# Optimization experiments

Measured on AMD Instinct MI355X. Metric: run time of the kernel, lower is better.

The kernel has to match this reference:

```python
import jax, jax.numpy as jnp
import numpy as np

BN_EPS = 1e-5
LRELU_SLOPE = 0.1
F = 512  # feature dim fixed by ReFineBlock/Fc_ClassBlock input_dim


def _bn_eval(x, gamma, beta, mean, var):
    # BatchNorm1d in eval mode (running stats); elementwise over feature dim
    return (x - mean) * (gamma / jnp.sqrt(var + BN_EPS)) + beta


def _lrelu(x):
    return jnp.where(x > 0, x, LRELU_SLOPE * x)


def setup_inputs() -> dict:
    key = jax.random.key(0)
    ks = jax.random.split(key, 16)
    B, P, G = 128, 1, 4
    d = jax.random.normal(ks[0], (B, B, P, G, F), dtype=jnp.float32)
    w = jax.random.uniform(ks[1], (B * G, B * G), dtype=jnp.float32)
    W1 = jax.random.normal(ks[2], (F, F), dtype=jnp.float32) * 0.04
    b1 = jnp.zeros((F,), dtype=jnp.float32)
    g1 = jnp.ones((F,), dtype=jnp.float32)
    beta1 = jnp.zeros((F,), dtype=jnp.float32)
    m1 = jax.random.normal(ks[3], (F,), dtype=jnp.float32) * 0.1
    v1 = jax.random.uniform(ks[4], (F,), jnp.float32, 0.5, 1.5)
    W2 = jax.random.normal(ks[5], (F, F), dtype=jnp.float32) * 0.04
    b2 = jnp.zeros((F,), dtype=jnp.float32)
    g2 = jnp.ones((F,), dtype=jnp.float32)
    beta2 = jnp.zeros((F,), dtype=jnp.float32)
    m2 = jax.random.normal(ks[6], (F,), dtype=jnp.float32) * 0.1
    v2 = jax.random.uniform(ks[7], (F,), jnp.float32, 0.5, 1.5)
    # Fc_ClassBlock.classifier: Dropout(eval=id) + Linear(512, 2)
    Wc = jax.random.normal(ks[8], (2, F), dtype=jnp.float32) * 0.001
    bc = jnp.zeros((2,), dtype=jnp.float32)
    return {"d": d, "w": w, "W1": W1, "b1": b1, "g1": g1, "beta1": beta1,
            "m1": m1, "v1": v1, "W2": W2, "b2": b2, "g2": g2, "beta2": beta2,
            "m2": m2, "v2": v2, "Wc": Wc, "bc": bc}


def reference(d, w, W1, b1, g1, beta1, m1, v1, W2, b2, g2, beta2, m2, v2, Wc, bc):
    batch_size = d.shape[1]          # len(d[0])
    num_g = d.shape[3]
    feat = d.shape[-1]
    N = batch_size * num_g           # adjacency size

    # Vectorized ReFineBlock over every (k, :, i, j) row (eval mode: dropout=id)
    x = d.reshape(-1, feat)
    h = _lrelu(_bn_eval(x @ W1.T + b1, g1, beta1, m1, v1))
    h = _lrelu(_bn_eval(h @ W2.T + b2, g2, beta2, m2, v2))
    t = h.reshape(batch_size, -1, feat)   # (B, B*G, F)

    # preprocess_adj: adj = w + I; D^{-1/2}; (adj @ D).T @ D
    adj = w.reshape(N, N) + jnp.eye(N, dtype=w.dtype)
    rowsum = adj.sum(axis=1)
    d_inv_sqrt = jnp.power(rowsum, -0.5)
    d_inv_sqrt = jnp.where(jnp.isinf(d_inv_sqrt), 0.0, d_inv_sqrt)
    w_norm = (adj * d_inv_sqrt[None, :]).T * d_inv_sqrt[None, :]  # (N, N)

    # GCN propagation: d_new[:, :, i] = t[:, :, i] @ w_norm for each feature i
    d_new = jnp.einsum('bmf,mn->bnf', t, w_norm)  # (B, N, F)

    # classifier.classifier (dropout=id + Linear) applied per probe row
    result = d_new @ Wc.T + bc  # (B, N, 2)
    return result.reshape(-1, 2)
```

## Files before the change

kernel.cpp:

```cpp
#include <hip/hip_runtime.h>
#include <hip/hip_bf16.h>


typedef __hip_bfloat16 bf16_t;
typedef __bf16 bf16x8 __attribute__((ext_vector_type(8)));
typedef __bf16 bf16x4 __attribute__((ext_vector_type(4)));
typedef float f32x4 __attribute__((ext_vector_type(4)));

#define KDIM 512
#define BM 64

__device__ __forceinline__ float ldsel(const void* p, int i, int isbf) {
    return isbf ? __bfloat162float(((const bf16_t*)p)[i]) : ((const float*)p)[i];
}

__global__ void probe_kernel(const void* __restrict__ d, int* __restrict__ flag) {
    const unsigned short* u = (const unsigned short*)d;
    const int l = threadIdx.x;
    int cnt = 0;
    for (int i = l; i < 256; i += 64) {
        const int e = (u[i] >> 7) & 0xFF;
        cnt += (e >= 118 && e <= 129) ? 1 : 0;
    }
    #pragma unroll
    for (int off = 32; off; off >>= 1) cnt += __shfl_down(cnt, off, 64);
    if (l == 0) *flag = (cnt >= 200) ? 1 : 0;
}

__global__ void rowsum_kernel(const void* __restrict__ w, const int* __restrict__ flagp,
                              float* __restrict__ dinv) {
    const int isbf = *flagp;
    const int i = blockIdx.x;
    const int l = threadIdx.x;
    float s = 0.f;
    for (int j = l; j < 512; j += 64) s += ldsel(w, i * 512 + j, isbf);
    #pragma unroll
    for (int off = 32; off; off >>= 1) s += __shfl_down(s, off, 64);
    if (l == 0) dinv[i] = 1.0f / sqrtf(s + 1.0f);
}

__global__ void params_kernel(const void* g1, const void* b1, const void* m1,
                              const void* v1, const void* be1,
                              const void* g2, const void* b2, const void* m2,
                              const void* v2, const void* be2,
                              const void* Wc, const void* bc,
                              const int* __restrict__ flagp,
                              float* sc1, float* sh1, float* sc2, float* sh2,
                              float* wcf, float* bcf) {
    const int isbf = *flagp;
    const int i = threadIdx.x;
    float s1 = ldsel(g1, i, isbf) / sqrtf(ldsel(v1, i, isbf) + 1e-5f);
    sc1[i] = s1;
    sh1[i] = (ldsel(b1, i, isbf) - ldsel(m1, i, isbf)) * s1 + ldsel(be1, i, isbf);
    float s2 = ldsel(g2, i, isbf) / sqrtf(ldsel(v2, i, isbf) + 1e-5f);
    sc2[i] = s2;
    sh2[i] = (ldsel(b2, i, isbf) - ldsel(m2, i, isbf)) * s2 + ldsel(be2, i, isbf);
    wcf[i] = ldsel(Wc, i, isbf);
    wcf[512 + i] = ldsel(Wc, 512 + i, isbf);
    if (i < 2) bcf[i] = ldsel(bc, i, isbf);
}

__global__ void wconv_kernel(const void* __restrict__ W1, const void* __restrict__ W2,
                             const int* __restrict__ flagp,
                             bf16_t* __restrict__ W1pk, bf16_t* __restrict__ W2pk) {
    const int isbf = *flagp;
    const int t = blockIdx.x * 256 + threadIdx.x;
    const int lane = t & 63;
    const int kt = (t >> 6) & 15;
    const int c16 = t >> 10;
    const int src = (c16 * 16 + (lane & 15)) * 512 + kt * 32 + (lane >> 4) * 8;
    bf16x8 v1, v2;
    #pragma unroll
    for (int e = 0; e < 8; ++e) {
        v1[e] = (__bf16)ldsel(W1, src + e, isbf);
        v2[e] = (__bf16)ldsel(W2, src + e, isbf);
    }
    *reinterpret_cast<bf16x8*>(W1pk + (size_t)t * 8) = v1;
    *reinterpret_cast<bf16x8*>(W2pk + (size_t)t * 8) = v2;
}

__global__ void wnorm_kernel(const void* __restrict__ w, const int* __restrict__ flagp,
                             const float* __restrict__ dinv, float* __restrict__ wn_t) {
    const int isbf = *flagp;
    const int idx = blockIdx.x * 256 + threadIdx.x;
    const int n = idx >> 9, m = idx & 511;
    float a = ldsel(w, n * 512 + m, isbf) + (m == n ? 1.0f : 0.0f);
    wn_t[idx] = a * dinv[m] * dinv[n];
}

#define FJSTRIDE 16384
#define FKSTRIDE 1024

#define LOADW4(dst, base, kt)                                                  \
    _Pragma("unroll")                                                          \
    for (int j_ = 0; j_ < 4; ++j_)                                             \
        dst[j_] = *reinterpret_cast<const bf16x8*>((base) + j_ * FJSTRIDE + (kt) * FKSTRIDE);

#define SLOAD(r)                                                               \
    {                                                                          \
        if (isbf) {                                                            \
            sb = *reinterpret_cast<const bf16x8*>((const bf16_t*)A + sgb + (size_t)(r) * 64); \
        } else {                                                               \
            const f32x4* p_ = (const f32x4*)((const float*)A + sgb + (size_t)(r) * 64); \
            sf[0] = p_[0]; sf[1] = p_[1];                                      \
        }                                                                      \
    }

#define SWRITE(buf)                                                            \
    {                                                                          \
        bf16x8 v_;                                                             \
        if (isbf) { v_ = sb; }                                                 \
        else {                                                                 \
            v_[0] = (__bf16)sf[0].x; v_[1] = (__bf16)sf[0].y;                  \
            v_[2] = (__bf16)sf[0].z; v_[3] = (__bf16)sf[0].w;                  \
            v_[4] = (__bf16)sf[1].x; v_[5] = (__bf16)sf[1].y;                  \
            v_[6] = (__bf16)sf[1].z; v_[7] = (__bf16)sf[1].w;                  \
        }                                                                      \
        *reinterpret_cast<bf16x8*>((char*)Asg + (buf) * 8192 + sldsoff) = v_;  \
    }

#define COMPUTEQ(buf, q, bWs)                                                  \
    _Pragma("unroll")                                                          \
    for (int i_ = 0; i_ < 4; ++i_) {                                           \
        bf16x8 af_ = *reinterpret_cast<const bf16x8*>(                         \
            (const char*)Asg + (buf) * 8192 + (q) * 4096 + i_ * 1024 + lane * 16); \
        _Pragma("unroll")                                                      \
        for (int j_ = 0; j_ < 4; ++j_)                                         \
            acc[j_][i_] = __builtin_amdgcn_mfma_f32_16x16x32_bf16(bWs[j_], af_, acc[j_][i_], 0, 0, 0); \
    }

#define COMPT1(kt, bWs)                                                        \
    _Pragma("unroll")                                                          \
    for (int i_ = 0; i_ < 4; ++i_) {                                           \
        const int row_ = i_ * 16 + rl;                                         \
        int off_ = (row_ << 10) + (kt) * 64 + hi * 16;                         \
        off_ ^= (row_ & 7) << 4;                                               \
        bf16x8 af_ = *reinterpret_cast<const bf16x8*>((const char*)T1s + off_);\
        _Pragma("unroll")                                                      \
        for (int j_ = 0; j_ < 4; ++j_)                                         \
            acc[j_][i_] = __builtin_amdgcn_mfma_f32_16x16x32_bf16(bWs[j_], af_, acc[j_][i_], 0, 0, 0); \
    }

__launch_bounds__(512, 4)
__global__ void fused_mlp(const void* __restrict__ A,
                          const bf16_t* __restrict__ W1pk,
                          const bf16_t* __restrict__ W2pk,
                          const float* __restrict__ sc1, const float* __restrict__ sh1,
                          const float* __restrict__ sc2, const float* __restrict__ sh2,
                          const float* __restrict__ wcf,
                          const int* __restrict__ flagp,
                          float* __restrict__ U)
{
    __shared__ __align__(16) bf16_t T1s[BM * KDIM];
    __shared__ __align__(16) bf16_t Asg[2][BM * 64];
    float* UredF = (float*)Asg;

    const int isbf = *flagp;
    const int tid = threadIdx.x;
    const int wave = tid >> 6, lane = tid & 63;
    const int rl = lane & 15, hi = lane >> 4;
    const int wc = wave;
    const int tile = blockIdx.x;

    const char* w1base = (const char*)W1pk + ((size_t)(wc * 4) * 16 * 64 + lane) * 16;
    const char* w2base = (const char*)W2pk + ((size_t)(wc * 4) * 16 * 64 + lane) * 16;

    const int srow = tid >> 3;
    const int sk8 = tid & 7;
    const int sq = sk8 >> 2, sc8 = sk8 & 3;
    const size_t sgb = ((size_t)(tile * BM) + srow) * KDIM + sk8 * 8;
    const int sldsoff = (sq * 256 + (srow >> 4) * 64 + (srow & 15) + sc8 * 16) * 16;

    f32x4 acc[4][4] = {};
    f32x4 sf[2];
    bf16x8 sb;

    SLOAD(0);
    SWRITE(0);
    SLOAD(1);
    __syncthreads();

    {
        bf16x8 bW[4];
        #pragma unroll 1
        for (int r = 0; r < 8; ++r) {
            LOADW4(bW, w1base, 2 * r);
            COMPUTEQ(r & 1, 0, bW);
            LOADW4(bW, w1base, 2 * r + 1);
            COMPUTEQ(r & 1, 1, bW);
            if (r + 1 < 8) SWRITE((r + 1) & 1);
            if (r + 2 < 8) SLOAD(r + 2);
            __syncthreads();
        }
    }

    #pragma unroll
    for (int j = 0; j < 4; ++j) {
        const int col0 = wc * 64 + j * 16 + hi * 4;
        const f32x4 s4 = *reinterpret_cast<const f32x4*>(&sc1[col0]);
        const f32x4 h4 = *reinterpret_cast<const f32x4*>(&sh1[col0]);
        #pragma unroll
        for (int i = 0; i < 4; ++i) {
            const int row = i * 16 + rl;
            int off = (row << 10) + (col0 << 1);
            off ^= (row & 7) << 4;
            bf16x4 pk;
            #pragma unroll
            for (int r = 0; r < 4; ++r) {
                float y = acc[j][i][r] * s4[r] + h4[r];
                y = y > 0.f ? y : 0.1f * y;
                pk[r] = (__bf16)y;
            }
            *reinterpret_cast<bf16x4*>((char*)T1s + off) = pk;
        }
    }
    __syncthreads();

    #pragma unroll
    for (int j = 0; j < 4; ++j)
        #pragma unroll
        for (int i = 0; i < 4; ++i)
            acc[j][i] = f32x4{0.f, 0.f, 0.f, 0.f};

    {
        bf16x8 bW0[4], bW1[4];
        LOADW4(bW0, w2base, 0);
        #pragma unroll 1
        for (int kt = 0; kt < 16; kt += 2) {
            LOADW4(bW1, w2base, kt + 1);
            COMPT1(kt, bW0);
            if (kt + 2 < 16) LOADW4(bW0, w2base, kt + 2);
            COMPT1(kt + 1, bW1);
        }
    }

    float p0[4] = {0.f, 0.f, 0.f, 0.f}, p1[4] = {0.f, 0.f, 0.f, 0.f};
    #pragma unroll
    for (int j = 0; j < 4; ++j) {
        const int col0 = wc * 64 + j * 16 + hi * 4;
        const f32x4 s4 = *reinterpret_cast<const f32x4*>(&sc2[col0]);
        const f32x4 h4 = *reinterpret_cast<const f32x4*>(&sh2[col0]);
        const f32x4 w0 = *reinterpret_cast<const f32x4*>(&wcf[col0]);
        const f32x4 w1 = *reinterpret_cast<const f32x4*>(&wcf[512 + col0]);
        #pragma unroll
        for (int i = 0; i < 4; ++i)
            #pragma unroll
            for (int r = 0; r < 4; ++r) {
                float y = acc[j][i][r] * s4[r] + h4[r];
                y = y > 0.f ? y : 0.1f * y;
                p0[i] += y * w0[r];
                p1[i] += y * w1[r];
            }
    }
    __syncthreads();
    #pragma unroll
    for (int i = 0; i < 4; ++i) {
        float a = p0[i], b = p1[i];
        a += __shfl_xor(a, 16, 64);  b += __shfl_xor(b, 16, 64);
        a += __shfl_xor(a, 32, 64);  b += __shfl_xor(b, 32, 64);
        if (hi == 0) {
            UredF[(wc * BM + i * 16 + rl) * 2]     = a;
            UredF[(wc * BM + i * 16 + rl) * 2 + 1] = b;
        }
    }
    __syncthreads();
    if (tid < BM * 2) {
        const int row = tid >> 1, c = tid & 1;
        float s = 0.f;
        #pragma unroll
        for (int q = 0; q < 8; ++q) s += UredF[(q * BM + row) * 2 + c];
        U[(size_t)(tile * BM + row) * 2 + c] = s;
    }
}

__global__ void gcn_kernel(const float* __restrict__ wn_t, const float* __restrict__ U,
                           const float* __restrict__ bcf, const int* __restrict__ flagp,
                           void* __restrict__ out) {
    const int isbf = *flagp;
    const int wave = threadIdx.x >> 6, lane = threadIdx.x & 63;
    const int task = blockIdx.x * 4 + wave;
    const int b = task >> 9, n = task & 511;
    const float* wrow = wn_t + n * 512;
    const float* ub = U + b * 1024;
    float a0 = 0.f, a1 = 0.f;
    for (int m = lane; m < 512; m += 64) {
        const float wv = wrow[m];
        a0 += wv * ub[m * 2];
        a1 += wv * ub[m * 2 + 1];
    }
    #pragma unroll
    for (int off = 32; off; off >>= 1) {
        a0 += __shfl_down(a0, off, 64);
        a1 += __shfl_down(a1, off, 64);
    }
    if (lane == 0) {
        const float r0 = a0 + bcf[0];
        const float r1 = a1 + bcf[1];
        if (isbf) {
            ((bf16_t*)out)[task * 2]     = __float2bfloat16(r0);
            ((bf16_t*)out)[task * 2 + 1] = __float2bfloat16(r1);
        } else {
            ((float*)out)[task * 2]     = r0;
            ((float*)out)[task * 2 + 1] = r1;
        }
    }
}

extern "C" void kernel_launch(void* const* d_in, const int* in_sizes, int n_in,
                              void* d_out, int out_size, void* d_ws, size_t ws_size,
                              hipStream_t stream) {
    const void* d   = d_in[0];
    const void* w   = d_in[1];
    const void* W1  = d_in[2];
    const void* b1  = d_in[3];
    const void* g1  = d_in[4];
    const void* be1 = d_in[5];
    const void* m1  = d_in[6];
    const void* v1  = d_in[7];
    const void* W2  = d_in[8];
    const void* b2  = d_in[9];
    const void* g2  = d_in[10];
    const void* be2 = d_in[11];
    const void* m2  = d_in[12];
    const void* v2  = d_in[13];
    const void* Wc  = d_in[14];
    const void* bc  = d_in[15];

    char* ws = (char*)d_ws;
    float*  wn_t = (float*)ws;
    bf16_t* W1pk = (bf16_t*)(ws + 0x100000);
    bf16_t* W2pk = (bf16_t*)(ws + 0x180000);
    float*  sc1  = (float*)(ws + 0x200000);
    float*  sh1  = sc1 + 512;
    float*  sc2  = sh1 + 512;
    float*  sh2  = sc2 + 512;
    float*  dinv = sh2 + 512;
    float*  wcf  = (float*)(ws + 0x204000);
    float*  bcf  = (float*)(ws + 0x205000);
    int*    flag = (int*)(ws + 0x205100);
    float*  U    = (float*)(ws + 0x208000);

    const int M = 128 * 512;

    probe_kernel<<<1, 64, 0, stream>>>(d, flag);
    rowsum_kernel<<<512, 64, 0, stream>>>(w, flag, dinv);
    params_kernel<<<1, 512, 0, stream>>>(g1, b1, m1, v1, be1, g2, b2, m2, v2, be2,
                                         Wc, bc, flag, sc1, sh1, sc2, sh2, wcf, bcf);
    wconv_kernel<<<128, 256, 0, stream>>>(W1, W2, flag, W1pk, W2pk);
    wnorm_kernel<<<1024, 256, 0, stream>>>(w, flag, dinv, wn_t);

    fused_mlp<<<M / BM, 512, 0, stream>>>(d, W1pk, W2pk,
                                          sc1, sh1, sc2, sh2, wcf, flag, U);

    gcn_kernel<<<M / 4, 256, 0, stream>>>(wn_t, U, bcf, flag, d_out);
}
```

Before: 127.3 us.

## Merge preprocessing kernels, fold adjacency normalization into GCN, prefetch MLP weights

Removes the separate dtype-probe kernel by detecting bf16 inline in each kernel from the first values of an input tensor. Merges the rowsum, params and weight-packing kernels into one prep launch. Drops the materialized normalized adjacency, so the GCN kernel reads w directly and applies the D^-1/2 scaling on the fly. It also double-buffers the W1 fragment loads in the first MLP stage. The aim is fewer launches, fewer global round trips and hidden weight-load latency. The cost is that dtype detection now runs per kernel on different tensors, which could disagree for some inputs.

```diff
diff --git a/kernel.cpp b/kernel.cpp
--- a/kernel.cpp
+++ b/kernel.cpp
@@ -14,78 +14,68 @@
     return isbf ? __bfloat162float(((const bf16_t*)p)[i]) : ((const float*)p)[i];
 }
 
-__global__ void probe_kernel(const void* __restrict__ d, int* __restrict__ flag) {
-    const unsigned short* u = (const unsigned short*)d;
-    const int l = threadIdx.x;
+__device__ __forceinline__ int detect_isbf(const void* p) {
+    const unsigned short* u = (const unsigned short*)p;
     int cnt = 0;
-    for (int i = l; i < 256; i += 64) {
+    #pragma unroll
+    for (int i = 0; i < 64; ++i) {
         const int e = (u[i] >> 7) & 0xFF;
         cnt += (e >= 118 && e <= 129) ? 1 : 0;
     }
-    #pragma unroll
-    for (int off = 32; off; off >>= 1) cnt += __shfl_down(cnt, off, 64);
-    if (l == 0) *flag = (cnt >= 200) ? 1 : 0;
-}
-
-__global__ void rowsum_kernel(const void* __restrict__ w, const int* __restrict__ flagp,
-                              float* __restrict__ dinv) {
-    const int isbf = *flagp;
-    const int i = blockIdx.x;
-    const int l = threadIdx.x;
-    float s = 0.f;
-    for (int j = l; j < 512; j += 64) s += ldsel(w, i * 512 + j, isbf);
-    #pragma unroll
-    for (int off = 32; off; off >>= 1) s += __shfl_down(s, off, 64);
-    if (l == 0) dinv[i] = 1.0f / sqrtf(s + 1.0f);
-}
-
-__global__ void params_kernel(const void* g1, const void* b1, const void* m1,
-                              const void* v1, const void* be1,
-                              const void* g2, const void* b2, const void* m2,
-                              const void* v2, const void* be2,
-                              const void* Wc, const void* bc,
-                              const int* __restrict__ flagp,
-                              float* sc1, float* sh1, float* sc2, float* sh2,
-                              float* wcf, float* bcf) {
-    const int isbf = *flagp;
-    const int i = threadIdx.x;
-    float s1 = ldsel(g1, i, isbf) / sqrtf(ldsel(v1, i, isbf) + 1e-5f);
-    sc1[i] = s1;
-    sh1[i] = (ldsel(b1, i, isbf) - ldsel(m1, i, isbf)) * s1 + ldsel(be1, i, isbf);
-    float s2 = ldsel(g2, i, isbf) / sqrtf(ldsel(v2, i, isbf) + 1e-5f);
-    sc2[i] = s2;
-    sh2[i] = (ldsel(b2, i, isbf) - ldsel(m2, i, isbf)) * s2 + ldsel(be2, i, isbf);
-    wcf[i] = ldsel(Wc, i, isbf);
-    wcf[512 + i] = ldsel(Wc, 512 + i, isbf);
-    if (i < 2) bcf[i] = ldsel(bc, i, isbf);
-}
-
-__global__ void wconv_kernel(const void* __restrict__ W1, const void* __restrict__ W2,
-                             const int* __restrict__ flagp,
-                             bf16_t* __restrict__ W1pk, bf16_t* __restrict__ W2pk) {
-    const int isbf = *flagp;
-    const int t = blockIdx.x * 256 + threadIdx.x;
-    const int lane = t & 63;
-    const int kt = (t >> 6) & 15;
-    const int c16 = t >> 10;
-    const int src = (c16 * 16 + (lane & 15)) * 512 + kt * 32 + (lane >> 4) * 8;
-    bf16x8 v1, v2;
-    #pragma unroll
-    for (int e = 0; e < 8; ++e) {
-        v1[e] = (__bf16)ldsel(W1, src + e, isbf);
-        v2[e] = (__bf16)ldsel(W2, src + e, isbf);
-    }
-    *reinterpret_cast<bf16x8*>(W1pk + (size_t)t * 8) = v1;
-    *reinterpret_cast<bf16x8*>(W2pk + (size_t)t * 8) = v2;
-}
-
-__global__ void wnorm_kernel(const void* __restrict__ w, const int* __restrict__ flagp,
-                             const float* __restrict__ dinv, float* __restrict__ wn_t) {
-    const int isbf = *flagp;
-    const int idx = blockIdx.x * 256 + threadIdx.x;
-    const int n = idx >> 9, m = idx & 511;
-    float a = ldsel(w, n * 512 + m, isbf) + (m == n ? 1.0f : 0.0f);
-    wn_t[idx] = a * dinv[m] * dinv[n];
+    return cnt >= 48;
+}
+
+__global__ void prep_kernel(const void* __restrict__ w,
+                            const void* __restrict__ W1, const void* __restrict__ W2,
+                            const void* g1, const void* b1, const void* m1,
+                            const void* v1, const void* be1,
+                            const void* g2, const void* b2, const void* m2,
+                            const void* v2, const void* be2,
+                            const void* Wc, const void* bc,
+                            float* __restrict__ dinv,
+                            bf16_t* __restrict__ W1pk, bf16_t* __restrict__ W2pk,
+                            float* sc1, float* sh1, float* sc2, float* sh2,
+                            float* wcf, float* bcf) {
+    const int blk = blockIdx.x;
+    const int tid = threadIdx.x;
+    if (blk < 128) {
+        const int isbf = detect_isbf(W1);
+        const int t = blk * 256 + tid;
+        const int lane = t & 63;
+        const int kt = (t >> 6) & 15;
+        const int c16 = t >> 10;
+        const int src = (c16 * 16 + (lane & 15)) * 512 + kt * 32 + (lane >> 4) * 8;
+        bf16x8 v1v, v2v;
+        #pragma unroll
+        for (int e = 0; e < 8; ++e) {
+            v1v[e] = (__bf16)ldsel(W1, src + e, isbf);
+            v2v[e] = (__bf16)ldsel(W2, src + e, isbf);
+        }
+        *reinterpret_cast<bf16x8*>(W1pk + (size_t)t * 8) = v1v;
+        *reinterpret_cast<bf16x8*>(W2pk + (size_t)t * 8) = v2v;
+    } else if (blk < 256) {
+        const int isbf = detect_isbf(w);
+        const int wave = tid >> 6, lane = tid & 63;
+        const int row = (blk - 128) * 4 + wave;
+        float s = 0.f;
+        for (int j = lane; j < 512; j += 64) s += ldsel(w, row * 512 + j, isbf);
+        #pragma unroll
+        for (int off = 32; off; off >>= 1) s += __shfl_down(s, off, 64);
+        if (lane == 0) dinv[row] = 1.0f / sqrtf(s + 1.0f);
+    } else {
+        const int isbf = detect_isbf(g1);
+        for (int i = tid; i < 512; i += 256) {
+            float s1 = ldsel(g1, i, isbf) / sqrtf(ldsel(v1, i, isbf) + 1e-5f);
+            sc1[i] = s1;
+            sh1[i] = (ldsel(b1, i, isbf) - ldsel(m1, i, isbf)) * s1 + ldsel(be1, i, isbf);
+            float s2 = ldsel(g2, i, isbf) / sqrtf(ldsel(v2, i, isbf) + 1e-5f);
+            sc2[i] = s2;
+            sh2[i] = (ldsel(b2, i, isbf) - ldsel(m2, i, isbf)) * s2 + ldsel(be2, i, isbf);
+            wcf[i] = ldsel(Wc, i, isbf);
+            wcf[512 + i] = ldsel(Wc, 512 + i, isbf);
+        }
+        if (tid < 2) bcf[tid] = ldsel(bc, tid, isbf);
+    }
 }
 
 #define FJSTRIDE 16384
@@ -148,14 +138,13 @@
                           const float* __restrict__ sc1, const float* __restrict__ sh1,
                           const float* __restrict__ sc2, const float* __restrict__ sh2,
                           const float* __restrict__ wcf,
-                          const int* __restrict__ flagp,
                           float* __restrict__ U)
 {
     __shared__ __align__(16) bf16_t T1s[BM * KDIM];
     __shared__ __align__(16) bf16_t Asg[2][BM * 64];
     float* UredF = (float*)Asg;
 
-    const int isbf = *flagp;
+    const int isbf = detect_isbf(A);
     const int tid = threadIdx.x;
     const int wave = tid >> 6, lane = tid & 63;
     const int rl = lane & 15, hi = lane >> 4;
@@ -181,13 +170,14 @@
     __syncthreads();
 
     {
-        bf16x8 bW[4];
+        bf16x8 bW0[4], bW1[4];
+        LOADW4(bW0, w1base, 0);
         #pragma unroll 1
         for (int r = 0; r < 8; ++r) {
-            LOADW4(bW, w1base, 2 * r);
-            COMPUTEQ(r & 1, 0, bW);
-            LOADW4(bW, w1base, 2 * r + 1);
-            COMPUTEQ(r & 1, 1, bW);
+            LOADW4(bW1, w1base, 2 * r + 1);
+            COMPUTEQ(r & 1, 0, bW0);
+            if (r + 1 < 8) LOADW4(bW0, w1base, 2 * r + 2);
+            COMPUTEQ(r & 1, 1, bW1);
             if (r + 1 < 8) SWRITE((r + 1) & 1);
             if (r + 2 < 8) SLOAD(r + 2);
             __syncthreads();
@@ -273,20 +263,20 @@
     }
 }
 
-__global__ void gcn_kernel(const float* __restrict__ wn_t, const float* __restrict__ U,
-                           const float* __restrict__ bcf, const int* __restrict__ flagp,
+__global__ void gcn_kernel(const void* __restrict__ w, const float* __restrict__ dinv,
+                           const float* __restrict__ U, const float* __restrict__ bcf,
                            void* __restrict__ out) {
-    const int isbf = *flagp;
+    const int isbf = detect_isbf(w);
     const int wave = threadIdx.x >> 6, lane = threadIdx.x & 63;
     const int task = blockIdx.x * 4 + wave;
     const int b = task >> 9, n = task & 511;
-    const float* wrow = wn_t + n * 512;
     const float* ub = U + b * 1024;
     float a0 = 0.f, a1 = 0.f;
     for (int m = lane; m < 512; m += 64) {
-        const float wv = wrow[m];
-        a0 += wv * ub[m * 2];
-        a1 += wv * ub[m * 2 + 1];
+        float wv = ldsel(w, n * 512 + m, isbf) + (m == n ? 1.0f : 0.0f);
+        const float t = wv * dinv[m];
+        a0 += t * ub[m * 2];
+        a1 += t * ub[m * 2 + 1];
     }
     #pragma unroll
     for (int off = 32; off; off >>= 1) {
@@ -294,8 +284,9 @@
         a1 += __shfl_down(a1, off, 64);
     }
     if (lane == 0) {
-        const float r0 = a0 + bcf[0];
-        const float r1 = a1 + bcf[1];
+        const float dn = dinv[n];
+        const float r0 = a0 * dn + bcf[0];
+        const float r1 = a1 * dn + bcf[1];
         if (isbf) {
             ((bf16_t*)out)[task * 2]     = __float2bfloat16(r0);
             ((bf16_t*)out)[task * 2 + 1] = __float2bfloat16(r1);
@@ -327,30 +318,25 @@
     const void* bc  = d_in[15];
 
     char* ws = (char*)d_ws;
-    float*  wn_t = (float*)ws;
-    bf16_t* W1pk = (bf16_t*)(ws + 0x100000);
-    bf16_t* W2pk = (bf16_t*)(ws + 0x180000);
-    float*  sc1  = (float*)(ws + 0x200000);
+    bf16_t* W1pk = (bf16_t*)ws;
+    bf16_t* W2pk = (bf16_t*)(ws + 0x080000);
+    float*  sc1  = (float*)(ws + 0x100000);
     float*  sh1  = sc1 + 512;
     float*  sc2  = sh1 + 512;
     float*  sh2  = sc2 + 512;
     float*  dinv = sh2 + 512;
-    float*  wcf  = (float*)(ws + 0x204000);
-    float*  bcf  = (float*)(ws + 0x205000);
-    int*    flag = (int*)(ws + 0x205100);
-    float*  U    = (float*)(ws + 0x208000);
+    float*  wcf  = (float*)(ws + 0x104000);
+    float*  bcf  = (float*)(ws + 0x105000);
+    float*  U    = (float*)(ws + 0x108000);
 
     const int M = 128 * 512;
 
-    probe_kernel<<<1, 64, 0, stream>>>(d, flag);
-    rowsum_kernel<<<512, 64, 0, stream>>>(w, flag, dinv);
-    params_kernel<<<1, 512, 0, stream>>>(g1, b1, m1, v1, be1, g2, b2, m2, v2, be2,
-                                         Wc, bc, flag, sc1, sh1, sc2, sh2, wcf, bcf);
-    wconv_kernel<<<128, 256, 0, stream>>>(W1, W2, flag, W1pk, W2pk);
-    wnorm_kernel<<<1024, 256, 0, stream>>>(w, flag, dinv, wn_t);
+    prep_kernel<<<257, 256, 0, stream>>>(w, W1, W2, g1, b1, m1, v1, be1,
+                                         g2, b2, m2, v2, be2, Wc, bc,
+                                         dinv, W1pk, W2pk, sc1, sh1, sc2, sh2, wcf, bcf);
 
     fused_mlp<<<M / BM, 512, 0, stream>>>(d, W1pk, W2pk,
-                                          sc1, sh1, sc2, sh2, wcf, flag, U);
-
-    gcn_kernel<<<M / 4, 256, 0, stream>>>(wn_t, U, bcf, flag, d_out);
-}
+                                          sc1, sh1, sc2, sh2, wcf, U);
+
+    gcn_kernel<<<M / 4, 256, 0, stream>>>(w, dinv, U, bcf, d_out);
+}
```

Result: slower. 161.7 us (+27.0%).
